# Kernel optimization log

Hardware: AMD Instinct MI355X
Metric: run time of the kernel (lower is better)

## Reference

```python
import jax, jax.numpy as jnp
import numpy as np


def conv2d(x, w, b=None, pad=1):
    out = jax.lax.conv_general_dilated(
        x, w, window_strides=(1, 1), padding=[(pad, pad), (pad, pad)],
        dimension_numbers=('NCHW', 'OIHW', 'NCHW'))
    if b is not None:
        out = out + b[None, :, None, None]
    return out


def instance_norm(x, eps=1e-5):
    # InstanceNorm2d (no affine): normalize each (b, c) plane over H, W (biased var)
    mu = x.mean(axis=(2, 3), keepdims=True)
    var = x.var(axis=(2, 3), keepdims=True)
    return (x - mu) * jax.lax.rsqrt(var + eps)


def setup_inputs() -> dict:
    key = jax.random.key(0)
    ks = jax.random.split(key, 16)
    B, C, H, W, F, L, NH = 4, 64, 128, 128, 5, 512, 128
    s = lambda i, shape: jax.random.normal(ks[i], shape, jnp.float32) * 0.05
    return {
        'x': jax.random.normal(ks[0], (B, C, H, W), jnp.float32),
        'segmap': jax.random.randint(ks[1], (B, F, H, W), 0, 2).astype(jnp.float32),
        'codes_vector': jax.random.normal(ks[2], (B, F, L), jnp.float32),
        'mask': jax.random.randint(ks[3], (B, 3, H, W), 0, 2).astype(jnp.float32),
        'fc_w': s(4, (F, L, L)),           # per facial-feature Linear weight [out,in]
        'fc_b': s(5, (F, L)),
        'conv_gamma_w': s(6, (C, L, 3, 3)),
        'conv_gamma_b': s(7, (C,)),
        'conv_beta_w': s(8, (C, L, 3, 3)),
        'conv_beta_b': s(9, (C,)),
        'spade_shared_w': s(10, (NH, 3, 3, 3)),
        'spade_shared_b': s(11, (NH,)),
        'spade_gamma_w': s(12, (C, NH, 3, 3)),
        'spade_gamma_b': s(13, (C,)),
        'spade_beta_w': s(14, (C, NH, 3, 3)),
        'spade_beta_b': s(15, (C,)),
        'blending_gamma': jnp.zeros((1,), jnp.float32),
        'blending_beta': jnp.zeros((1,), jnp.float32),
    }


def reference(x, segmap, codes_vector, mask, fc_w, fc_b,
              conv_gamma_w, conv_gamma_b, conv_beta_w, conv_beta_b,
              spade_shared_w, spade_shared_b, spade_gamma_w, spade_gamma_b,
              spade_beta_w, spade_beta_b, blending_gamma, blending_beta):
    B, C, H, W = x.shape
    F_ = segmap.shape[1]
    x_norm = instance_norm(x)  # add_noise=False branch
    seg_bool = segmap > 0      # [B, F, H, W]; segmap already at x resolution
    # per-region style vector: mu[b,f,:] = relu(Linear_f(codes_vector[b,f]))
    mu = jax.nn.relu(jnp.einsum('bfl,fkl->bfk', codes_vector, fc_w) + fc_b[None])  # [B,F,L]
    # vectorized replacement of the per-(b,j) masked_scatter_ loop: later regions overwrite
    L = mu.shape[-1]
    middle = jnp.zeros((B, L, H, W), x.dtype)
    for j in range(F_):
        middle = jnp.where(seg_bool[:, j][:, None], mu[:, j][:, :, None, None], middle)
    gamma_avg = conv2d(middle, conv_gamma_w, conv_gamma_b)
    beta_avg = conv2d(middle, conv_beta_w, conv_beta_b)
    # SPADE on the (already full-res) mask
    actv = jax.nn.relu(conv2d(mask, spade_shared_w, spade_shared_b))
    gamma_spade = conv2d(actv, spade_gamma_w, spade_gamma_b)
    beta_spade = conv2d(actv, spade_beta_w, spade_beta_b)
    ga = jax.nn.sigmoid(blending_gamma)[0]
    ba = jax.nn.sigmoid(blending_beta)[0]
    gamma_final = ga * gamma_avg + (1.0 - ga) * gamma_spade
    beta_final = ba * beta_avg + (1.0 - ba) * beta_spade
    return x_norm * (1.0 + gamma_final) + beta_final
```

## Files before the change

### kernel.cpp

```cpp
#include <hip/hip_runtime.h>
#include <math.h>

#define HD 128
#define WD 128
#define LD 512
#define NHD 128
#define HW (HD*WD)

typedef _Float16 half8 __attribute__((ext_vector_type(8)));
typedef float floatx4 __attribute__((ext_vector_type(4)));
typedef float floatx16 __attribute__((ext_vector_type(16)));

#define OFF_MU      0
#define OFF_TG      10240
#define OFF_TB      24064
#define OFF_MEAN    37888
#define OFF_RSTD    38144
#define OFF_CT      38400
#define OFF_W3      628224
#define OFF_ACTVH   701952
#define OFF_IDX_BYTES ((size_t)(701952 + 4194304) * 4)

__global__ void __launch_bounds__(256) k_pre1(
    const float* __restrict__ x, const float* __restrict__ segmap,
    const float* __restrict__ codes, const float* __restrict__ mask,
    const float* __restrict__ fc_w, const float* __restrict__ fc_b,
    const float* __restrict__ cgw, const float* __restrict__ cbw,
    const float* __restrict__ sgw, const float* __restrict__ sbw,
    const float* __restrict__ ssw, const float* __restrict__ ssb,
    const float* __restrict__ bgam, const float* __restrict__ bbet,
    float* __restrict__ mu, float* __restrict__ CT, _Float16* __restrict__ W3,
    unsigned char* __restrict__ idxm, float* __restrict__ meanp,
    float* __restrict__ rstdp, _Float16* __restrict__ actvh) {
    int bid = blockIdx.x, t = threadIdx.x;

    if (bid < 256) {
        __shared__ float sl[64][37];
        int tbl = bid >> 7, cq4 = bid & 127;
        const float* src = tbl ? cbw : cgw;
        int o = t >> 2, q = t & 3;
        const float* sp = src + (size_t)o * 4608 + cq4 * 36 + q * 9;
        #pragma unroll
        for (int j = 0; j < 9; ++j) sl[o][q * 9 + j] = sp[j];
        __syncthreads();
        int o_w = t & 63, s = t >> 6;
        float* dst = CT + (size_t)tbl * 294912;
        #pragma unroll
        for (int tap = 0; tap < 9; ++tap)
            dst[((size_t)tap * 512 + cq4 * 4 + s) * 64 + o_w] = sl[o_w][s * 9 + tap];
        return;
    }
    if (bid < 288) {
        __shared__ _Float16 sl2[32][145];
        int e2 = bid - 256;
        int tbl = e2 >> 4, ocg = (e2 >> 3) & 1, chq = e2 & 7;
        const float* src = tbl ? sbw : sgw;
        float blg = 1.f / (1.f + __expf(-bgam[0]));
        float blb = 1.f / (1.f + __expf(-bbet[0]));
        float scale = tbl ? (1.f - blb) : (1.f - blg);
        int oc_r = t >> 3, i = t & 7;
        const float* sp = src + (size_t)(ocg * 32 + oc_r) * 1152 + chq * 144 + i * 18;
        #pragma unroll
        for (int j = 0; j < 18; ++j) sl2[oc_r][i * 18 + j] = (_Float16)(sp[j] * scale);
        __syncthreads();
        for (int s = 0; s < 3; ++s) {
            int task = s * 256 + t;
            if (task < 576) {
                int tap = task >> 6, ln = task & 63;
                int lo = ln & 31, hb = ln >> 5;
                half8 hv;
                #pragma unroll
                for (int j = 0; j < 8; ++j)
                    hv[j] = sl2[lo][(hb * 8 + j) * 9 + tap];
                *(half8*)(W3 + ((((size_t)tbl * 9 + tap) * 2 + ocg) * 8 + chq) * 512
                          + ln * 8) = hv;
            }
        }
        return;
    }
    if (bid < 448) {
        __shared__ float cs[LD];
        int sid = bid - 288;
        int bf = sid >> 3, chunk = sid & 7, f = bf % 5;
        cs[t] = codes[(size_t)bf * LD + t];
        cs[t + 256] = codes[(size_t)bf * LD + t + 256];
        __syncthreads();
        int row = t >> 2, lane4 = t & 3;
        int k = chunk * 64 + row;
        const float* wrow = fc_w + ((size_t)f * LD + k) * LD;
        float acc = 0.f;
        for (int j = 0; j < 32; ++j) {
            int l = lane4 * 4 + j * 16;
            float4 wv = *(const float4*)(wrow + l);
            float4 cv = *(const float4*)(cs + l);
            acc += wv.x * cv.x + wv.y * cv.y + wv.z * cv.z + wv.w * cv.w;
        }
        acc += __shfl_xor(acc, 1);
        acc += __shfl_xor(acc, 2);
        if (lane4 == 0)
            mu[(size_t)bf * LD + k] = fmaxf(acc + fc_b[f * LD + k], 0.f);
        return;
    }
    if (bid < 704) {
        int pid = (bid - 448) * 256 + t;
        int b = pid >> 14, p = pid & 16383;
        unsigned char v = 5;
        for (int f = 0; f < 5; ++f)
            if (segmap[((size_t)b * 5 + f) * HW + p] > 0.f) v = (unsigned char)f;
        idxm[pid] = v;
        return;
    }
    if (bid < 960) {
        __shared__ float as[4], as2[4];
        int plane = bid - 704;
        const float* xp = x + (size_t)plane * HW;
        float s = 0.f, s2 = 0.f;
        for (int j = 0; j < 16; ++j) {
            float4 v = *(const float4*)(xp + ((size_t)t + j * 256) * 4);
            s += v.x + v.y + v.z + v.w;
            s2 += v.x * v.x + v.y * v.y + v.z * v.z + v.w * v.w;
        }
        for (int off = 32; off; off >>= 1) { s += __shfl_xor(s, off); s2 += __shfl_xor(s2, off); }
        int wid = t >> 6;
        if ((t & 63) == 0) { as[wid] = s; as2[wid] = s2; }
        __syncthreads();
        if (t == 0) {
            s = as[0] + as[1] + as[2] + as[3];
            s2 = as2[0] + as2[1] + as2[2] + as2[3];
            float m = s * (1.f / HW);
            float var = s2 * (1.f / HW) - m * m;
            meanp[plane] = m;
            rstdp[plane] = rsqrtf(var + 1e-5f);
        }
        return;
    }
    {
        __shared__ float ml[3][3][66];
        __shared__ float wl[NHD * 27];
        __shared__ float bl[NHD];
        int sid = bid - 960;
        int xh = sid & 1, h = (sid >> 1) & 127, b = sid >> 8;
        int w0 = xh * 64;
        for (int e = t; e < NHD * 27; e += 256) wl[e] = ssw[e];
        if (t < NHD) bl[t] = ssb[t];
        for (int e = t; e < 594; e += 256) {
            int col = e % 66; int rc = e / 66; int ky = rc % 3; int c = rc / 3;
            int y = h - 1 + ky; int xx = w0 - 1 + col;
            float v = 0.f;
            if ((unsigned)y < 128u && (unsigned)xx < 128u)
                v = mask[(((size_t)b * 3 + c) * HD + y) * WD + xx];
            ml[c][ky][col] = v;
        }
        __syncthreads();
        int n = t & 127, wh = t >> 7;
        const float* wn = wl + n * 27;
        _Float16* outp = actvh + ((((size_t)b * HD + h) * WD) + w0 + wh * 32) * NHD + n;
        for (int i = 0; i < 32; ++i) {
            int pcol = wh * 32 + i;
            float acc = bl[n];
            #pragma unroll
            for (int c = 0; c < 3; ++c)
                #pragma unroll
                for (int ky = 0; ky < 3; ++ky)
                    #pragma unroll
                    for (int kx = 0; kx < 3; ++kx)
                        acc = fmaf(ml[c][ky][pcol + kx], wn[(c * 3 + ky) * 3 + kx], acc);
            outp[(size_t)i * NHD] = (_Float16)fmaxf(acc, 0.f);
        }
    }
}

__global__ void __launch_bounds__(1024) k_pre2(
    const float* __restrict__ mu, const float* __restrict__ CT,
    float* __restrict__ Tg, float* __restrict__ Tb) {
    int bid = blockIdx.x;
    int tap = bid % 9; int bf6 = bid / 9;
    int f = bf6 % 6, b = bf6 / 6;
    int t = threadIdx.x;
    size_t base = (size_t)bid * 64;
    if (f == 5) {
        if (t < 64) { Tg[base + t] = 0.f; Tb[base + t] = 0.f; }
        return;
    }
    __shared__ float ms[LD];
    __shared__ float red[2][16][64];
    if (t < 512) ms[t] = mu[(((size_t)b * 5 + f) << 9) + t];
    __syncthreads();
    int o = t & 63, cq = t >> 6;
    const float* cg = CT + ((size_t)tap * 512 + cq * 32) * 64 + o;
    const float* cb = cg + 294912;
    float ag = 0.f, ab = 0.f;
    #pragma unroll 8
    for (int i = 0; i < 32; ++i) {
        float m = ms[cq * 32 + i];
        ag = fmaf(m, cg[(size_t)i * 64], ag);
        ab = fmaf(m, cb[(size_t)i * 64], ab);
    }
    red[0][cq][o] = ag; red[1][cq][o] = ab;
    __syncthreads();
    if (t < 128) {
        int tb2 = t >> 6, oo = t & 63;
        float s = 0.f;
        #pragma unroll
        for (int i = 0; i < 16; ++i) s += red[tb2][i][oo];
        (tb2 ? Tb : Tg)[base + oo] = s;
    }
}

__global__ void __launch_bounds__(512, 4)
k_main(const float* __restrict__ x, const _Float16* __restrict__ actvh,
       const unsigned char* __restrict__ idxm,
       const float* __restrict__ Tg, const float* __restrict__ Tb,
       const _Float16* __restrict__ W3,
       const float* __restrict__ meanp, const float* __restrict__ rstdp,
       const float* __restrict__ cgb, const float* __restrict__ cbb,
       const float* __restrict__ sgb, const float* __restrict__ sbb,
       const float* __restrict__ bgam, const float* __restrict__ bbet,
       float* __restrict__ out) {
    __shared__ _Float16 As[4 * 66 * 64];
    __shared__ _Float16 T2f[8192];
    __shared__ unsigned char ir[4][68];
    int t = threadIdx.x;

    int gid = blockIdx.x;
    int logical = (gid & 7) * 64 + (gid >> 3);
    int c64 = logical & 1, rp = (logical >> 1) & 63, b = logical >> 7;
    int w0 = c64 * 64, y0 = rp * 2;

    int lane = t & 63, w = t >> 6;
    int pxg = w >> 1, ocg = w & 1;
    int row_l = pxg >> 1, c32 = (pxg & 1) * 32;
    int l31 = lane & 31, hi = lane >> 5;

    float ga = 1.f / (1.f + __expf(-bgam[0]));
    float ba = 1.f / (1.f + __expf(-bbet[0]));

    if (t < 264) {
        int r = t / 66, j = t % 66;
        int y = y0 - 1 + r, xx = w0 + j - 1;
        ir[r][j] = ((unsigned)y < 128u && (unsigned)xx < 128u)
                       ? idxm[((size_t)b << 14) + (y << 7) + xx] : (unsigned char)5;
    }
    for (int task = t; task < 1024; task += 512) {
        int tbl = task >> 9, rem = task & 511;
        int ocs = rem >> 8, ks = (rem >> 6) & 3, ln = rem & 63;
        int oc = ocs * 32 + (ln & 31);
        int kb = ks * 16 + (ln >> 5) * 8;
        const float* Tsrc = tbl ? Tb : Tg;
        float sc = tbl ? ba : ga;
        half8 hv;
        #pragma unroll
        for (int j = 0; j < 8; ++j) {
            int k = kb + j;
            int f = (k * 57) >> 9;
            int tp = k - f * 9;
            float v = (f < 6) ? Tsrc[(((size_t)b * 6 + f) * 9 + tp) * 64 + oc] * sc : 0.f;
            hv[j] = (_Float16)v;
        }
        *(half8*)(&T2f[task * 8]) = hv;
    }

    floatx16 accg, accb;
    #pragma unroll
    for (int i = 0; i < 16; ++i) { accg[i] = 0.f; accb[i] = 0.f; }

    for (int half = 0; half < 2; ++half) {
        int ch0 = half * 64;
        for (int e = t; e < 2112; e += 512) {
            int ch8 = e & 7, col = (e >> 3) % 66, row = e / 528;
            int y = y0 - 1 + row, xx = w0 - 1 + col;
            uint4 v = make_uint4(0u, 0u, 0u, 0u);
            if ((unsigned)y < 128u && (unsigned)xx < 128u)
                v = *(const uint4*)(actvh + ((((size_t)b * HD + y) * WD + xx) << 7)
                                    + ch0 + ch8 * 8);
            *(uint4*)(&As[((row * 66 + col) << 6) + ((ch8 ^ (col & 7)) << 3)]) = v;
        }
        __syncthreads();
        #pragma unroll
        for (int tap = 0; tap < 9; ++tap) {
            int ky = tap / 3, kx = tap - ky * 3;
            int colA = c32 + l31 + kx;
            int rowA = row_l + ky;
            int abase = (rowA * 66 + colA) << 6;
            int sw = colA & 7;
            const _Float16* wg = W3 + ((((size_t)tap) * 2 + ocg) * 8 + half * 4) * 512
                                 + lane * 8;
            const _Float16* wb2 = wg + (size_t)9 * 2 * 8 * 512;
            #pragma unroll
            for (int ks = 0; ks < 4; ++ks) {
                half8 a = *(const half8*)(&As[abase + (((ks * 2 + hi) ^ sw) << 3)]);
                half8 bg = *(const half8*)(wg + ks * 512);
                half8 bb = *(const half8*)(wb2 + ks * 512);
                accg = __builtin_amdgcn_mfma_f32_32x32x16_f16(a, bg, accg, 0, 0, 0);
                accb = __builtin_amdgcn_mfma_f32_32x32x16_f16(a, bb, accb, 0, 0, 0);
            }
        }
        __syncthreads();
    }

    unsigned long long fpack = 0ull;
    #pragma unroll
    for (int ky = 0; ky < 3; ++ky)
        #pragma unroll
        for (int kx = 0; kx < 3; ++kx) {
            unsigned long long f = ir[row_l + ky][c32 + l31 + kx];
            fpack |= f << ((ky * 3 + kx) * 6);
        }
    #pragma unroll
    for (int ks = 0; ks < 4; ++ks) {
        int kb = ks * 16 + hi * 8;
        half8 a1;
        #pragma unroll
        for (int j = 0; j < 8; ++j) {
            int k = kb + j;
            int f = (k * 57) >> 9;
            int tp6 = (k - f * 9) * 6;
            int fp = (int)((fpack >> tp6) & 63ull);
            a1[j] = (fp == f) ? (_Float16)1.0f : (_Float16)0.0f;
        }
        half8 bg = *(const half8*)(&T2f[(((0 * 2 + ocg) * 4 + ks) * 64 + lane) * 8]);
        half8 bb = *(const half8*)(&T2f[(((2 + ocg) * 4 + ks) * 64 + lane) * 8]);
        accg = __builtin_amdgcn_mfma_f32_32x32x16_f16(a1, bg, accg, 0, 0, 0);
        accb = __builtin_amdgcn_mfma_f32_32x32x16_f16(a1, bb, accb, 0, 0, 0);
    }

    int oc = ocg * 32 + l31;
    int plane = b * 64 + oc;
    float mean = meanp[plane], rstd = rstdp[plane];
    float gbias = ga * cgb[oc] + (1.f - ga) * sgb[oc];
    float bbias = ba * cbb[oc] + (1.f - ba) * sbb[oc];
    size_t rowoff = (size_t)plane * HW + (y0 + row_l) * WD + w0 + c32;
    const float* xrow = x + rowoff;
    float* orow = out + rowoff;
    #pragma unroll
    for (int q = 0; q < 4; ++q) {
        int p0 = 8 * q + 4 * hi;
        float4 xv = *(const float4*)(xrow + p0);
        float xa[4] = {xv.x, xv.y, xv.z, xv.w};
        float res[4];
        #pragma unroll
        for (int r2 = 0; r2 < 4; ++r2) {
            float gf = accg[q * 4 + r2] + gbias;
            float bf = accb[q * 4 + r2] + bbias;
            res[r2] = (xa[r2] - mean) * rstd * (1.f + gf) + bf;
        }
        *(float4*)(orow + p0) = make_float4(res[0], res[1], res[2], res[3]);
    }
}

extern "C" void kernel_launch(void* const* d_in, const int* in_sizes, int n_in,
                              void* d_out, int out_size, void* d_ws, size_t ws_size,
                              hipStream_t stream) {
    const float* x      = (const float*)d_in[0];
    const float* segmap = (const float*)d_in[1];
    const float* codes  = (const float*)d_in[2];
    const float* mask   = (const float*)d_in[3];
    const float* fc_w   = (const float*)d_in[4];
    const float* fc_b   = (const float*)d_in[5];
    const float* cgw    = (const float*)d_in[6];
    const float* cgb    = (const float*)d_in[7];
    const float* cbw    = (const float*)d_in[8];
    const float* cbb    = (const float*)d_in[9];
    const float* ssw    = (const float*)d_in[10];
    const float* ssb    = (const float*)d_in[11];
    const float* sgw    = (const float*)d_in[12];
    const float* sgb    = (const float*)d_in[13];
    const float* sbw    = (const float*)d_in[14];
    const float* sbb    = (const float*)d_in[15];
    const float* bgam   = (const float*)d_in[16];
    const float* bbet   = (const float*)d_in[17];
    float* out = (float*)d_out;

    float* wsf = (float*)d_ws;
    float* mu    = wsf + OFF_MU;
    float* Tg    = wsf + OFF_TG;
    float* Tb    = wsf + OFF_TB;
    float* meanp = wsf + OFF_MEAN;
    float* rstdp = wsf + OFF_RSTD;
    float* CT    = wsf + OFF_CT;
    _Float16* W3    = (_Float16*)(wsf + OFF_W3);
    _Float16* actvh = (_Float16*)(wsf + OFF_ACTVH);
    unsigned char* idxm = (unsigned char*)d_ws + OFF_IDX_BYTES;

    k_pre1<<<1984, 256, 0, stream>>>(x, segmap, codes, mask, fc_w, fc_b,
                                     cgw, cbw, sgw, sbw, ssw, ssb, bgam, bbet,
                                     mu, CT, W3, idxm, meanp, rstdp, actvh);
    k_pre2<<<216, 1024, 0, stream>>>(mu, CT, Tg, Tb);
    k_main<<<512, 512, 0, stream>>>(x, actvh, idxm, Tg, Tb, W3,
                                    meanp, rstdp, cgb, cbb, sgb, sbb,
                                    bgam, bbet, out);
}
```

Measured before the change: 161.8 us.

## Use MFMA for SPADE shared conv and widen k_main waves to both channel groups

The 3-channel SPADE shared conv in k_pre1 moves from per-thread scalar FMA loops to MFMA 32x32x16 f16 tiles, with the K=27 dimension padded to 32. Results are staged in a shared buffer so actvh rows are written with coalesced half8 stores. k_main drops from 512 to 256 threads per block, and each wave now computes both 32-channel output groups, so every A fragment read from shared memory feeds four MFMAs instead of two. The cost is double the accumulator registers per wave and fewer waves per block to hide latency. The new A-fragment code also contains a redundant dead load expression.

```diff
diff --git a/kernel.cpp b/kernel.cpp
--- a/kernel.cpp
+++ b/kernel.cpp
@@ -20,6 +20,10 @@
 #define OFF_W3      628224
 #define OFF_ACTVH   701952
 #define OFF_IDX_BYTES ((size_t)(701952 + 4194304) * 4)
+
+__device__ constexpr int mloff(int k) {
+    return ((k / 9) * 3 + ((k % 9) / 3)) * 66 + ((k % 9) % 3);
+}
 
 __global__ void __launch_bounds__(256) k_pre1(
     const float* __restrict__ x, const float* __restrict__ segmap,
@@ -136,13 +140,11 @@
     }
     {
         __shared__ float ml[3][3][66];
-        __shared__ float wl[NHD * 27];
-        __shared__ float bl[NHD];
+        __shared__ _Float16 Bs2[4096];
+        __shared__ _Float16 Cbuf[8192];
         int sid = bid - 960;
         int xh = sid & 1, h = (sid >> 1) & 127, b = sid >> 8;
         int w0 = xh * 64;
-        for (int e = t; e < NHD * 27; e += 256) wl[e] = ssw[e];
-        if (t < NHD) bl[t] = ssb[t];
         for (int e = t; e < 594; e += 256) {
             int col = e % 66; int rc = e / 66; int ky = rc % 3; int c = rc / 3;
             int y = h - 1 + ky; int xx = w0 - 1 + col;
@@ -151,21 +153,61 @@
                 v = mask[(((size_t)b * 3 + c) * HD + y) * WD + xx];
             ml[c][ky][col] = v;
         }
-        __syncthreads();
-        int n = t & 127, wh = t >> 7;
-        const float* wn = wl + n * 27;
-        _Float16* outp = actvh + ((((size_t)b * HD + h) * WD) + w0 + wh * 32) * NHD + n;
-        for (int i = 0; i < 32; ++i) {
-            int pcol = wh * 32 + i;
-            float acc = bl[n];
+        for (int e = t; e < 512; e += 256) {
+            int ks = e >> 8, hb = (e >> 7) & 1, oc = e & 127;
+            int kb = ks * 16 + hb * 8;
+            half8 hv;
             #pragma unroll
-            for (int c = 0; c < 3; ++c)
+            for (int j = 0; j < 8; ++j)
+                hv[j] = (kb + j < 27) ? (_Float16)ssw[oc * 27 + kb + j] : (_Float16)0.f;
+            *(half8*)(&Bs2[(size_t)e * 8]) = hv;
+        }
+        __syncthreads();
+        int lane = t & 63, wv = t >> 6;
+        int l31 = lane & 31, hb = lane >> 5;
+        int oc = wv * 32 + l31;
+        const float* mlf = &ml[0][0][0];
+        floatx16 acc[2];
+        #pragma unroll
+        for (int i = 0; i < 16; ++i) { acc[0][i] = 0.f; acc[1][i] = 0.f; }
+        #pragma unroll
+        for (int ks = 0; ks < 2; ++ks) {
+            half8 bfrag = *(const half8*)(&Bs2[((ks * 2 + hb) * 128 + oc) * 8]);
+            #pragma unroll
+            for (int mf = 0; mf < 2; ++mf) {
+                int px = mf * 32 + l31;
+                half8 a;
                 #pragma unroll
-                for (int ky = 0; ky < 3; ++ky)
-                    #pragma unroll
-                    for (int kx = 0; kx < 3; ++kx)
-                        acc = fmaf(ml[c][ky][pcol + kx], wn[(c * 3 + ky) * 3 + kx], acc);
-            outp[(size_t)i * NHD] = (_Float16)fmaxf(acc, 0.f);
+                for (int j = 0; j < 8; ++j) {
+                    int k_lo = ks * 16 + j;
+                    int k_hi = k_lo + 8;
+                    float v;
+                    if (k_hi < 27)
+                        v = mlf[(hb ? mloff(18 + (k_lo - (k_lo / 9) * 9) + ((k_lo / 9) == 0 ? -9 : -9)) : 0) + 0];
+                    if (k_hi < 27)
+                        v = hb ? mlf[mloff(k_hi) + px] : mlf[mloff(k_lo) + px];
+                    else
+                        v = hb ? 0.f : mlf[mloff(k_lo) + px];
+                    a[j] = (_Float16)v;
+                }
+                acc[mf] = __builtin_amdgcn_mfma_f32_32x32x16_f16(a, bfrag, acc[mf], 0, 0, 0);
+            }
+        }
+        float bv = ssb[oc];
+        #pragma unroll
+        for (int mf = 0; mf < 2; ++mf)
+            #pragma unroll
+            for (int q = 0; q < 4; ++q)
+                #pragma unroll
+                for (int r = 0; r < 4; ++r) {
+                    int px = mf * 32 + 8 * q + 4 * hb + r;
+                    Cbuf[px * 128 + oc] = (_Float16)fmaxf(acc[mf][q * 4 + r] + bv, 0.f);
+                }
+        __syncthreads();
+        for (int e = t; e < 1024; e += 256) {
+            int px = e >> 4, ch8 = e & 15;
+            *(half8*)(actvh + (((size_t)b * HD + h) * WD + w0 + px) * NHD + ch8 * 8) =
+                *(const half8*)(&Cbuf[px * 128 + ch8 * 8]);
         }
     }
 }
@@ -207,7 +249,7 @@
     }
 }
 
-__global__ void __launch_bounds__(512, 4)
+__global__ void __launch_bounds__(256, 3)
 k_main(const float* __restrict__ x, const _Float16* __restrict__ actvh,
        const unsigned char* __restrict__ idxm,
        const float* __restrict__ Tg, const float* __restrict__ Tb,
@@ -228,20 +270,19 @@
     int w0 = c64 * 64, y0 = rp * 2;
 
     int lane = t & 63, w = t >> 6;
-    int pxg = w >> 1, ocg = w & 1;
-    int row_l = pxg >> 1, c32 = (pxg & 1) * 32;
+    int row_l = w >> 1, c32 = (w & 1) * 32;
     int l31 = lane & 31, hi = lane >> 5;
 
     float ga = 1.f / (1.f + __expf(-bgam[0]));
     float ba = 1.f / (1.f + __expf(-bbet[0]));
 
-    if (t < 264) {
-        int r = t / 66, j = t % 66;
+    for (int e = t; e < 264; e += 256) {
+        int r = e / 66, j = e % 66;
         int y = y0 - 1 + r, xx = w0 + j - 1;
         ir[r][j] = ((unsigned)y < 128u && (unsigned)xx < 128u)
                        ? idxm[((size_t)b << 14) + (y << 7) + xx] : (unsigned char)5;
     }
-    for (int task = t; task < 1024; task += 512) {
+    for (int task = t; task < 1024; task += 256) {
         int tbl = task >> 9, rem = task & 511;
         int ocs = rem >> 8, ks = (rem >> 6) & 3, ln = rem & 63;
         int oc = ocs * 32 + (ln & 31);
@@ -260,13 +301,16 @@
         *(half8*)(&T2f[task * 8]) = hv;
     }
 
-    floatx16 accg, accb;
+    floatx16 accg[2], accb[2];
     #pragma unroll
-    for (int i = 0; i < 16; ++i) { accg[i] = 0.f; accb[i] = 0.f; }
+    for (int i = 0; i < 16; ++i) {
+        accg[0][i] = 0.f; accg[1][i] = 0.f;
+        accb[0][i] = 0.f; accb[1][i] = 0.f;
+    }
 
     for (int half = 0; half < 2; ++half) {
         int ch0 = half * 64;
-        for (int e = t; e < 2112; e += 512) {
+        for (int e = t; e < 2112; e += 256) {
             int ch8 = e & 7, col = (e >> 3) % 66, row = e / 528;
             int y = y0 - 1 + row, xx = w0 - 1 + col;
             uint4 v = make_uint4(0u, 0u, 0u, 0u);
@@ -283,16 +327,21 @@
             int rowA = row_l + ky;
             int abase = (rowA * 66 + colA) << 6;
             int sw = colA & 7;
-            const _Float16* wg = W3 + ((((size_t)tap) * 2 + ocg) * 8 + half * 4) * 512
-                                 + lane * 8;
-            const _Float16* wb2 = wg + (size_t)9 * 2 * 8 * 512;
+            const _Float16* wg0 = W3 + (((size_t)tap * 2 + 0) * 8 + half * 4) * 512
+                                  + lane * 8;
+            const _Float16* wg1 = W3 + (((size_t)tap * 2 + 1) * 8 + half * 4) * 512
+                                  + lane * 8;
             #pragma unroll
             for (int ks = 0; ks < 4; ++ks) {
                 half8 a = *(const half8*)(&As[abase + (((ks * 2 + hi) ^ sw) << 3)]);
-                half8 bg = *(const half8*)(wg + ks * 512);
-                half8 bb = *(const half8*)(wb2 + ks * 512);
-                accg = __builtin_amdgcn_mfma_f32_32x32x16_f16(a, bg, accg, 0, 0, 0);
-                accb = __builtin_amdgcn_mfma_f32_32x32x16_f16(a, bb, accb, 0, 0, 0);
+                half8 bg0 = *(const half8*)(wg0 + ks * 512);
+                half8 bg1 = *(const half8*)(wg1 + ks * 512);
+                half8 bb0 = *(const half8*)(wg0 + 73728 + ks * 512);
+                half8 bb1 = *(const half8*)(wg1 + 73728 + ks * 512);
+                accg[0] = __builtin_amdgcn_mfma_f32_32x32x16_f16(a, bg0, accg[0], 0, 0, 0);
+                accg[1] = __builtin_amdgcn_mfma_f32_32x32x16_f16(a, bg1, accg[1], 0, 0, 0);
+                accb[0] = __builtin_amdgcn_mfma_f32_32x32x16_f16(a, bb0, accb[0], 0, 0, 0);
+                accb[1] = __builtin_amdgcn_mfma_f32_32x32x16_f16(a, bb1, accb[1], 0, 0, 0);
             }
         }
         __syncthreads();
@@ -318,33 +367,39 @@
             int fp = (int)((fpack >> tp6) & 63ull);
             a1[j] = (fp == f) ? (_Float16)1.0f : (_Float16)0.0f;
         }
-        half8 bg = *(const half8*)(&T2f[(((0 * 2 + ocg) * 4 + ks) * 64 + lane) * 8]);
-        half8 bb = *(const half8*)(&T2f[(((2 + ocg) * 4 + ks) * 64 + lane) * 8]);
-        accg = __builtin_amdgcn_mfma_f32_32x32x16_f16(a1, bg, accg, 0, 0, 0);
-        accb = __builtin_amdgcn_mfma_f32_32x32x16_f16(a1, bb, accb, 0, 0, 0);
-    }
-
-    int oc = ocg * 32 + l31;
-    int plane = b * 64 + oc;
-    float mean = meanp[plane], rstd = rstdp[plane];
-    float gbias = ga * cgb[oc] + (1.f - ga) * sgb[oc];
-    float bbias = ba * cbb[oc] + (1.f - ba) * sbb[oc];
-    size_t rowoff = (size_t)plane * HW + (y0 + row_l) * WD + w0 + c32;
-    const float* xrow = x + rowoff;
-    float* orow = out + rowoff;
+        #pragma unroll
+        for (int ocg = 0; ocg < 2; ++ocg) {
+            half8 bg = *(const half8*)(&T2f[((ocg * 4 + ks) * 64 + lane) * 8]);
+            half8 bb = *(const half8*)(&T2f[(((2 + ocg) * 4 + ks) * 64 + lane) * 8]);
+            accg[ocg] = __builtin_amdgcn_mfma_f32_32x32x16_f16(a1, bg, accg[ocg], 0, 0, 0);
+            accb[ocg] = __builtin_amdgcn_mfma_f32_32x32x16_f16(a1, bb, accb[ocg], 0, 0, 0);
+        }
+    }
+
     #pragma unroll
-    for (int q = 0; q < 4; ++q) {
-        int p0 = 8 * q + 4 * hi;
-        float4 xv = *(const float4*)(xrow + p0);
-        float xa[4] = {xv.x, xv.y, xv.z, xv.w};
-        float res[4];
-        #pragma unroll
-        for (int r2 = 0; r2 < 4; ++r2) {
-            float gf = accg[q * 4 + r2] + gbias;
-            float bf = accb[q * 4 + r2] + bbias;
-            res[r2] = (xa[r2] - mean) * rstd * (1.f + gf) + bf;
-        }
-        *(float4*)(orow + p0) = make_float4(res[0], res[1], res[2], res[3]);
+    for (int ocg = 0; ocg < 2; ++ocg) {
+        int oc = ocg * 32 + l31;
+        int plane = b * 64 + oc;
+        float mean = meanp[plane], rstd = rstdp[plane];
+        float gbias = ga * cgb[oc] + (1.f - ga) * sgb[oc];
+        float bbias = ba * cbb[oc] + (1.f - ba) * sbb[oc];
+        size_t rowoff = (size_t)plane * HW + (y0 + row_l) * WD + w0 + c32;
+        const float* xrow = x + rowoff;
+        float* orow = out + rowoff;
+        #pragma unroll
+        for (int q = 0; q < 4; ++q) {
+            int p0 = 8 * q + 4 * hi;
+            float4 xv = *(const float4*)(xrow + p0);
+            float xa[4] = {xv.x, xv.y, xv.z, xv.w};
+            float res[4];
+            #pragma unroll
+            for (int r2 = 0; r2 < 4; ++r2) {
+                float gf = accg[ocg][q * 4 + r2] + gbias;
+                float bf = accb[ocg][q * 4 + r2] + bbias;
+                res[r2] = (xa[r2] - mean) * rstd * (1.f + gf) + bf;
+            }
+            *(float4*)(orow + p0) = make_float4(res[0], res[1], res[2], res[3]);
+        }
     }
 }
 
@@ -386,7 +441,7 @@
                                      cgw, cbw, sgw, sbw, ssw, ssb, bgam, bbet,
                                      mu, CT, W3, idxm, meanp, rstdp, actvh);
     k_pre2<<<216, 1024, 0, stream>>>(mu, CT, Tg, Tb);
-    k_main<<<512, 512, 0, stream>>>(x, actvh, idxm, Tg, Tb, W3,
+    k_main<<<512, 256, 0, stream>>>(x, actvh, idxm, Tg, Tb, W3,
                                     meanp, rstdp, cgb, cbb, sgb, sbb,
                                     bgam, bbet, out);
 }
```

New measurement: 178.1 us. 1.1x slower.
